# Optimization experiments

Measured on AMD Instinct MI355X. Metric: run time of the kernel, lower is better.

The kernel has to match this reference:

```python
import jax, jax.numpy as jnp
import numpy as np

N_NODES = 100000
N_EDGES = 1600000
D = 128          # h_size == feature_representation_size
N_CLASSES = 2
N_GRAPHS = 64


def setup_inputs() -> dict:
    key = jax.random.key(0)
    ks = jax.random.split(key, 8)
    scale = 1.0 / np.sqrt(D)
    x = jax.random.normal(ks[0], (N_NODES, D), jnp.float32)
    edge_index = jax.random.randint(ks[1], (2, N_EDGES), 0, N_NODES, dtype=jnp.int64)
    batch = jnp.sort(jax.random.randint(ks[2], (N_NODES,), 0, N_GRAPHS, dtype=jnp.int64))
    W0 = jax.random.normal(ks[3], (D, D), jnp.float32) * scale
    W1 = jax.random.normal(ks[4], (D, D), jnp.float32) * scale
    W2 = jax.random.normal(ks[5], (D, D), jnp.float32) * scale
    Wf = jax.random.normal(ks[6], (D, N_CLASSES), jnp.float32) * scale
    return dict(
        x=x, edge_index=edge_index, batch=batch,
        W0=W0, b0=jnp.zeros((D,), jnp.float32),
        W1=W1, b1=jnp.zeros((D,), jnp.float32),
        W2=W2, b2=jnp.zeros((D,), jnp.float32),
        Wf=Wf, bf=jnp.zeros((N_CLASSES,), jnp.float32),
    )


def gcn_norm(edge_index, num_nodes):
    # add self loops, symmetric normalization D^{-1/2} A_hat D^{-1/2}
    src, dst = edge_index[0], edge_index[1]
    loop = jnp.arange(num_nodes, dtype=src.dtype)
    src = jnp.concatenate([src, loop])
    dst = jnp.concatenate([dst, loop])
    ew = jnp.ones(src.shape[0], jnp.float32)
    deg = jax.ops.segment_sum(ew, dst, num_segments=num_nodes)
    dinv = jnp.where(deg > 0, jax.lax.rsqrt(deg), 0.0)
    norm = dinv[src] * dinv[dst]  # [E+N]
    return src, dst, norm


def gcn_conv(h, W, b, src, dst, norm, num_nodes):
    h = h @ W                                   # linear transform
    msg = h[src] * norm[:, None]                # gather + scale over edges
    out = jax.ops.segment_sum(msg, dst, num_segments=num_nodes)  # scatter-add
    return out + b


def reference(x, edge_index, batch, W0, b0, W1, b1, W2, b2, Wf, bf):
    n = x.shape[0]
    src, dst, norm = gcn_norm(edge_index, n)
    h = jax.nn.relu(gcn_conv(x, W0, b0, src, dst, norm, n))
    h = jax.nn.relu(gcn_conv(h, W1, b1, src, dst, norm, n))
    h = gcn_conv(h, W2, b2, src, dst, norm, n)  # last layer, no relu
    pooled = jax.ops.segment_max(h, batch, num_segments=N_GRAPHS)  # global max pool
    return pooled @ Wf + bf
```

## Files before the change

kernel.cpp:

```cpp
#include <hip/hip_runtime.h>
#include <hip/hip_bf16.h>
#include <hip/hip_fp16.h>
#include <float.h>

#define D 128
#define NGRAPHS 64
#define BKSHIFT 9
#define BKNODES 512
#define MAXBK 256
#define PCH 2048

typedef _Float16 h8 __attribute__((ext_vector_type(8)));
typedef float f4 __attribute__((ext_vector_type(4)));

__device__ __forceinline__ unsigned fkey(float f){
  unsigned u = __float_as_uint(f);
  return (u & 0x80000000u) ? ~u : (u | 0x80000000u);
}
__device__ __forceinline__ float funkey(unsigned k){
  unsigned u = (k & 0x80000000u) ? (k ^ 0x80000000u) : ~k;
  return __uint_as_float(u);
}

__device__ __forceinline__ void wcvt_pair(const float* __restrict__ W,
    _Float16* __restrict__ dstp, int pair, int lane){
  int quad = lane >> 4;
  int n    = lane & 15;
  int k0 = pair >> 3;
  int tt = pair & 7;
  _Float16 v[8];
  #pragma unroll
  for (int j = 0; j < 8; j++){
    int k = k0 * 32 + quad * 8 + j;
    v[j] = (_Float16)W[k * 128 + 16 * tt + n];
  }
  *(uint4*)&dstp[((size_t)pair * 64 + lane) * 8] = *(uint4*)v;
}

__global__ __launch_bounds__(256) void k_wcvt0(const float* __restrict__ W0,
    _Float16* __restrict__ Wsw, int* __restrict__ bcnt){
  if (blockIdx.x == 0 && threadIdx.x < MAXBK) bcnt[threadIdx.x] = 0;
  int lane = threadIdx.x & 63;
  int pair = blockIdx.x * 4 + (threadIdx.x >> 6);
  wcvt_pair(W0, Wsw, pair, lane);
}

#define HCH 4096
__global__ __launch_bounds__(256) void k_mega(
    const float* __restrict__ x, const _Float16* __restrict__ Wsw0,
    _Float16* __restrict__ C, int M, int gb,
    const int* __restrict__ dst, int* __restrict__ bcnt, int E, int nh,
    const float* __restrict__ W1, const float* __restrict__ W2,
    _Float16* __restrict__ Wsw12){
  __shared__ __align__(16) char smraw[4 * 16 * 136 * 2];
  int bid = blockIdx.x;
  if (bid < gb){
    _Float16 (*lds)[136] = (_Float16(*)[136])(smraw + (threadIdx.x >> 6) * 16 * 136 * 2);
    int lane = threadIdx.x & 63;
    int quad = lane >> 4;
    int l15  = lane & 15;
    int m0 = bid * 64 + (threadIdx.x >> 6) * 16;
    if (m0 >= M) return;
    f4 acc[8] = {};
    h8 af[4];
    const float* arow = x + (size_t)(m0 + l15) * D;
    #pragma unroll
    for (int k0 = 0; k0 < 4; k0++){
      float4 a = *(const float4*)&arow[k0 * 32 + quad * 8];
      float4 b = *(const float4*)&arow[k0 * 32 + quad * 8 + 4];
      __half2 p0 = __floats2half2_rn(a.x, a.y);
      __half2 p1 = __floats2half2_rn(a.z, a.w);
      __half2 p2 = __floats2half2_rn(b.x, b.y);
      __half2 p3 = __floats2half2_rn(b.z, b.w);
      union { uint4 u; h8 v; } cv;
      cv.u.x = *(unsigned*)&p0; cv.u.y = *(unsigned*)&p1;
      cv.u.z = *(unsigned*)&p2; cv.u.w = *(unsigned*)&p3;
      af[k0] = cv.v;
    }
    #pragma unroll
    for (int k0 = 0; k0 < 4; k0++){
      #pragma unroll
      for (int t = 0; t < 8; t++){
        h8 bf = *(const h8*)&Wsw0[((size_t)(k0 * 8 + t) * 64 + lane) * 8];
        acc[t] = __builtin_amdgcn_mfma_f32_16x16x32_f16(af[k0], bf, acc[t], 0, 0, 0);
      }
    }
    #pragma unroll
    for (int t = 0; t < 8; t++){
      #pragma unroll
      for (int r = 0; r < 4; r++)
        lds[quad * 4 + r][t * 16 + l15] = (_Float16)acc[t][r];
    }
    #pragma unroll
    for (int it = 0; it < 4; it++){
      int idx = it * 64 + lane;
      int row = idx >> 4;
      int ch  = idx & 15;
      *(uint4*)&C[(size_t)(m0 + row) * D + ch * 8] = *(uint4*)&lds[row][ch * 8];
    }
    return;
  }
  bid -= gb;
  if (bid < nh){
    int* h = (int*)smraw;
    int t = threadIdx.x;
    for (int i = t; i < MAXBK; i += 256) h[i] = 0;
    __syncthreads();
    int e0 = bid * HCH;
    #pragma unroll
    for (int j = 0; j < HCH / 256; j++){
      int e = e0 + t + j * 256;
      if (e < E) atomicAdd(&h[dst[e] >> BKSHIFT], 1);
    }
    __syncthreads();
    for (int i = t; i < MAXBK; i += 256) if (h[i]) atomicAdd(&bcnt[i], h[i]);
    return;
  }
  bid -= nh;
  const float* W = (bid < 2) ? W1 : W2;
  _Float16* dstp = Wsw12 + ((bid < 2) ? 0 : 16384);
  int pbase = (bid & 1) * 16;
  int lane = threadIdx.x & 63;
  for (int pp = (threadIdx.x >> 6); pp < 16; pp += 4)
    wcvt_pair(W, dstp, pbase + pp, lane);
}

__global__ __launch_bounds__(256) void k_bscan(const int* __restrict__ bcnt,
    int* __restrict__ bOff, int* __restrict__ bCur, int* __restrict__ row_ptr,
    unsigned* __restrict__ pk, int nbk, int N, int E){
  __shared__ int sh[256];
  int t = threadIdx.x;
  for (int i = t; i < NGRAPHS * D; i += 256) pk[i] = 0u;
  int v = (t < nbk) ? bcnt[t] : 0;
  sh[t] = v; __syncthreads();
  for (int off = 1; off < 256; off <<= 1){
    int x = (t >= off) ? sh[t - off] : 0;
    __syncthreads();
    sh[t] += x;
    __syncthreads();
  }
  if (t < nbk){ int ex = sh[t] - v; bOff[t] = ex; bCur[t] = ex; }
  if (t == 0){ bOff[nbk] = E; row_ptr[N] = E; }
}

__global__ __launch_bounds__(256) void k_part(const int* __restrict__ src,
    const int* __restrict__ dst, int* __restrict__ bCur,
    uint2* __restrict__ epart, int E){
  __shared__ int scnt[MAXBK], soff[MAXBK], sbase[MAXBK], scur[MAXBK];
  __shared__ int stmp[256];
  __shared__ uint2 stage[PCH];
  int t = threadIdx.x;
  int e0 = blockIdx.x * PCH;
  int eN = E - e0; if (eN > PCH) eN = PCH;
  for (int i = t; i < MAXBK; i += 256){ scnt[i] = 0; scur[i] = 0; }
  __syncthreads();
  uint2 mye[PCH / 256];
  #pragma unroll
  for (int j = 0; j < PCH / 256; j++){
    int e = e0 + t + j * 256;
    if (e < E){
      mye[j].x = (unsigned)src[e];
      mye[j].y = (unsigned)dst[e];
      atomicAdd(&scnt[mye[j].y >> BKSHIFT], 1);
    }
  }
  __syncthreads();
  int v = scnt[t];
  stmp[t] = v; __syncthreads();
  for (int off = 1; off < 256; off <<= 1){
    int x = (t >= off) ? stmp[t - off] : 0;
    __syncthreads();
    stmp[t] += x;
    __syncthreads();
  }
  soff[t] = stmp[t] - v;
  if (v > 0) sbase[t] = atomicAdd(&bCur[t], v);
  __syncthreads();
  #pragma unroll
  for (int j = 0; j < PCH / 256; j++){
    int e = e0 + t + j * 256;
    if (e < E){
      int b = mye[j].y >> BKSHIFT;
      int l = atomicAdd(&scur[b], 1);
      stage[soff[b] + l] = mye[j];
    }
  }
  __syncthreads();
  for (int j = t; j < eN; j += 256){
    uint2 ed = stage[j];
    int b = (int)(ed.y >> BKSHIFT);
    epart[(size_t)sbase[b] + (j - soff[b])] = ed;
  }
}

__global__ __launch_bounds__(256) void k_bfill(const uint2* __restrict__ epart,
    const int* __restrict__ bOff, int* __restrict__ row_ptr,
    int* __restrict__ col, float* __restrict__ dinv, int N){
  __shared__ int hc[BKNODES], off[BKNODES], cur[BKNODES];
  __shared__ int stmp[256];
  int b = blockIdx.x, t = threadIdx.x;
  int base = bOff[b], cntE = bOff[b + 1] - base;
  int node0 = b << BKSHIFT;
  int nloc = N - node0; if (nloc > BKNODES) nloc = BKNODES;
  for (int i = t; i < BKNODES; i += 256) hc[i] = 0;
  __syncthreads();
  for (int j = t; j < cntE; j += 256){
    uint2 ed = epart[(size_t)base + j];
    atomicAdd(&hc[ed.y - node0], 1);
  }
  __syncthreads();
  int a0 = hc[2 * t], a1 = hc[2 * t + 1];
  int s = a0 + a1;
  stmp[t] = s; __syncthreads();
  for (int o = 1; o < 256; o <<= 1){
    int x = (t >= o) ? stmp[t - o] : 0;
    __syncthreads();
    stmp[t] += x;
    __syncthreads();
  }
  int ex = stmp[t] - s;
  off[2 * t] = ex; off[2 * t + 1] = ex + a0;
  __syncthreads();
  for (int i = t; i < nloc; i += 256){
    row_ptr[node0 + i] = base + off[i];
    dinv[node0 + i]    = rsqrtf((float)hc[i] + 1.0f);
    cur[i] = off[i];
  }
  __syncthreads();
  for (int j = t; j < cntE; j += 256){
    uint2 ed = epart[(size_t)base + j];
    int p = atomicAdd(&cur[ed.y - node0], 1);
    col[base + p] = (int)ed.x;
  }
}

__global__ __launch_bounds__(256) void gemm_mfma(const _Float16* __restrict__ A,
    const _Float16* __restrict__ Wsw, _Float16* __restrict__ C, int M){
  __shared__ _Float16 lds[4][16][136];
  int wave = threadIdx.x >> 6;
  int lane = threadIdx.x & 63;
  int quad = lane >> 4;
  int l15  = lane & 15;
  int m0 = blockIdx.x * 64 + wave * 16;
  if (m0 >= M) return;
  f4 acc[8] = {};
  h8 af[4];
  const _Float16* arow = A + (size_t)(m0 + l15) * D;
  #pragma unroll
  for (int k0 = 0; k0 < 4; k0++)
    af[k0] = *(const h8*)&arow[k0 * 32 + quad * 8];
  #pragma unroll
  for (int k0 = 0; k0 < 4; k0++){
    #pragma unroll
    for (int t = 0; t < 8; t++){
      h8 bf = *(const h8*)&Wsw[((size_t)(k0 * 8 + t) * 64 + lane) * 8];
      acc[t] = __builtin_amdgcn_mfma_f32_16x16x32_f16(af[k0], bf, acc[t], 0, 0, 0);
    }
  }
  #pragma unroll
  for (int t = 0; t < 8; t++){
    #pragma unroll
    for (int r = 0; r < 4; r++)
      lds[wave][quad * 4 + r][t * 16 + l15] = (_Float16)acc[t][r];
  }
  #pragma unroll
  for (int it = 0; it < 4; it++){
    int idx = it * 64 + lane;
    int row = idx >> 4;
    int ch  = idx & 15;
    *(uint4*)&C[(size_t)(m0 + row) * D + ch * 8] = *(uint4*)&lds[wave][row][ch * 8];
  }
}

__device__ __forceinline__ void accm(float* acc, uint4 u, float w){
  union { uint4 u; _Float16 h[8]; } cv;
  cv.u = u;
  #pragma unroll
  for (int k = 0; k < 8; k++)
    acc[k] += (float)cv.h[k] * w;
}

__global__ __launch_bounds__(256) void k_agg(const __half* __restrict__ t,
    const int* __restrict__ row_ptr, const int* __restrict__ col,
    const float* __restrict__ dinv, const float* __restrict__ bias,
    __half* __restrict__ outh, int relu, int N){
  int node = blockIdx.x * 4 + (threadIdx.x >> 6);
  if (node >= N) return;
  int lane = threadIdx.x & 63;
  int way  = lane >> 4;
  int cg   = (lane & 15) * 8;
  float di = dinv[node];
  int beg = row_ptr[node], end = row_ptr[node + 1];
  float acc[8] = {0.f,0.f,0.f,0.f,0.f,0.f,0.f,0.f};
  int j = beg + way;
  for (; j + 12 < end; j += 16){
    int s0 = col[j], s1 = col[j + 4], s2 = col[j + 8], s3 = col[j + 12];
    float w0 = dinv[s0] * di;
    float w1 = dinv[s1] * di;
    float w2 = dinv[s2] * di;
    float w3 = dinv[s3] * di;
    uint4 u0 = *(const uint4*)&t[(size_t)s0 * D + cg];
    uint4 u1 = *(const uint4*)&t[(size_t)s1 * D + cg];
    uint4 u2 = *(const uint4*)&t[(size_t)s2 * D + cg];
    uint4 u3 = *(const uint4*)&t[(size_t)s3 * D + cg];
    accm(acc, u0, w0);
    accm(acc, u1, w1);
    accm(acc, u2, w2);
    accm(acc, u3, w3);
  }
  for (; j < end; j += 4){
    int s = col[j];
    float w = dinv[s] * di;
    uint4 u = *(const uint4*)&t[(size_t)s * D + cg];
    accm(acc, u, w);
  }
  #pragma unroll
  for (int k = 0; k < 8; k++){
    acc[k] += __shfl_xor(acc[k], 16, 64);
    acc[k] += __shfl_xor(acc[k], 32, 64);
  }
  if (way == 0){
    uint4 su = *(const uint4*)&t[(size_t)node * D + cg];
    union { uint4 u; _Float16 h[8]; } sv; sv.u = su;
    float dii = di * di;
    float4 b0 = *(const float4*)&bias[cg];
    float4 b1 = *(const float4*)&bias[cg + 4];
    float bb[8] = {b0.x, b0.y, b0.z, b0.w, b1.x, b1.y, b1.z, b1.w};
    float o[8];
    #pragma unroll
    for (int k = 0; k < 8; k++)
      o[k] = acc[k] + (float)sv.h[k] * dii + bb[k];
    if (relu){
      #pragma unroll
      for (int k = 0; k < 8; k++) o[k] = fmaxf(o[k], 0.f);
    }
    __half2 p0 = __floats2half2_rn(o[0], o[1]);
    __half2 p1 = __floats2half2_rn(o[2], o[3]);
    __half2 p2 = __floats2half2_rn(o[4], o[5]);
    __half2 p3 = __floats2half2_rn(o[6], o[7]);
    uint4 u;
    u.x = *(unsigned*)&p0; u.y = *(unsigned*)&p1;
    u.z = *(unsigned*)&p2; u.w = *(unsigned*)&p3;
    *(uint4*)&outh[(size_t)node * D + cg] = u;
  }
}

__global__ __launch_bounds__(128) void k_pool(const __half* __restrict__ h,
    const int* __restrict__ batch, unsigned* __restrict__ pk, int N){
  int d = threadIdx.x;
  int n0 = blockIdx.x * 64;
  int nEnd = n0 + 64; if (nEnd > N) nEnd = N;
  float cur = -FLT_MAX;
  int curg = batch[n0];
  int n = n0;
  for (; n + 3 < nEnd; n += 4){
    const __half* r = &h[(size_t)n * D + d];
    __half v0 = r[0], v1 = r[D], v2 = r[2 * D], v3 = r[3 * D];
    int g0 = batch[n], g1 = batch[n + 1], g2 = batch[n + 2], g3 = batch[n + 3];
    if (g0 != curg){ atomicMax(&pk[curg * D + d], fkey(cur)); cur = -FLT_MAX; curg = g0; }
    cur = fmaxf(cur, __half2float(v0));
    if (g1 != curg){ atomicMax(&pk[curg * D + d], fkey(cur)); cur = -FLT_MAX; curg = g1; }
    cur = fmaxf(cur, __half2float(v1));
    if (g2 != curg){ atomicMax(&pk[curg * D + d], fkey(cur)); cur = -FLT_MAX; curg = g2; }
    cur = fmaxf(cur, __half2float(v2));
    if (g3 != curg){ atomicMax(&pk[curg * D + d], fkey(cur)); cur = -FLT_MAX; curg = g3; }
    cur = fmaxf(cur, __half2float(v3));
  }
  for (; n < nEnd; n++){
    int g = batch[n];
    if (g != curg){ atomicMax(&pk[curg * D + d], fkey(cur)); cur = -FLT_MAX; curg = g; }
    cur = fmaxf(cur, __half2float(h[(size_t)n * D + d]));
  }
  atomicMax(&pk[curg * D + d], fkey(cur));
}

__global__ __launch_bounds__(128) void k_final(const unsigned* __restrict__ pk,
    const float* __restrict__ Wf, const float* __restrict__ bf,
    float* __restrict__ out){
  int t = threadIdx.x;
  int g = t >> 1, c = t & 1;
  float s = bf[c];
  for (int k = 0; k < D; k++)
    s += funkey(pk[g * D + k]) * Wf[k * 2 + c];
  out[g * 2 + c] = s;
}

extern "C" void kernel_launch(void* const* d_in, const int* in_sizes, int n_in,
                              void* d_out, int out_size, void* d_ws, size_t ws_size,
                              hipStream_t stream){
  const float* x   = (const float*)d_in[0];
  const int*   ei  = (const int*)d_in[1];
  const int*   bat = (const int*)d_in[2];
  const float* W0  = (const float*)d_in[3];
  const float* b0  = (const float*)d_in[4];
  const float* W1  = (const float*)d_in[5];
  const float* b1  = (const float*)d_in[6];
  const float* W2  = (const float*)d_in[7];
  const float* b2  = (const float*)d_in[8];
  const float* Wf  = (const float*)d_in[9];
  const float* bf  = (const float*)d_in[10];
  int N = in_sizes[0] / D;
  int E = in_sizes[1] / 2;
  const int* srcp = ei;
  const int* dstp = ei + E;
  int nbk   = (N + BKNODES - 1) / BKNODES;
  int npart = (E + PCH - 1) / PCH;
  int nh    = (E + HCH - 1) / HCH;
  int gb    = (N + 63) / 64;

  char* p = (char*)d_ws;
  auto alloc = [&](size_t bytes)->char*{
    char* r = p; p += (bytes + 255) & ~(size_t)255; return r;
  };
  float*     dinv    = (float*)alloc((size_t)N * 4);
  int*       row_ptr = (int*)alloc((size_t)(N + 1) * 4);
  int*       col     = (int*)alloc((size_t)E * 4);
  uint2*     epart   = (uint2*)alloc((size_t)E * 8);
  _Float16*  tmp     = (_Float16*)alloc((size_t)N * D * 2);
  _Float16*  tmp2    = (_Float16*)alloc((size_t)N * D * 2);
  _Float16*  Wsw     = (_Float16*)alloc((size_t)3 * 16384 * 2);
  unsigned*  pk      = (unsigned*)alloc((size_t)NGRAPHS * D * 4);
  int*       bcnt    = (int*)alloc((size_t)MAXBK * 4);
  int*       bOff    = (int*)alloc((size_t)(MAXBK + 1) * 4);
  int*       bCur    = (int*)alloc((size_t)MAXBK * 4);

  k_wcvt0<<<8, 256, 0, stream>>>(W0, Wsw, bcnt);
  k_mega<<<gb + nh + 4, 256, 0, stream>>>(x, Wsw, tmp, N, gb,
      dstp, bcnt, E, nh, W1, W2, Wsw + 16384);
  k_bscan<<<1, 256, 0, stream>>>(bcnt, bOff, bCur, row_ptr, pk, nbk, N, E);
  k_part<<<npart, 256, 0, stream>>>(srcp, dstp, bCur, epart, E);
  k_bfill<<<nbk, 256, 0, stream>>>(epart, bOff, row_ptr, col, dinv, N);

  int ablocks = (N + 3) / 4;
  k_agg<<<ablocks, 256, 0, stream>>>((const __half*)tmp, row_ptr, col, dinv, b0, (__half*)tmp2, 1, N);
  gemm_mfma<<<gb, 256, 0, stream>>>(tmp2, Wsw + 16384, tmp, N);
  k_agg<<<ablocks, 256, 0, stream>>>((const __half*)tmp, row_ptr, col, dinv, b1, (__half*)tmp2, 1, N);
  gemm_mfma<<<gb, 256, 0, stream>>>(tmp2, Wsw + 32768, tmp, N);
  k_agg<<<ablocks, 256, 0, stream>>>((const __half*)tmp, row_ptr, col, dinv, b2, (__half*)tmp2, 0, N);
  k_pool<<<(N + 63) / 64, 128, 0, stream>>>((const __half*)tmp2, bat, pk, N);
  k_final<<<1, 128, 0, stream>>>(pk, Wf, bf, (float*)d_out);
}
```

Before: 411.1 us.

## Fuse aggregation with the next layer's MFMA transform and fuse max-pooling

Layers 2 and 3 now aggregate neighbours first and then multiply by the weight matrix inside one kernel. Each wave aggregates 16 nodes into LDS, runs the MFMA GEMM, and applies bias and ReLU. The final layer max-pools straight from LDS instead of writing the hidden state, which removes the separate GEMM and pool kernels and two full N×D fp16 round trips. The cost is that each wave walks its 16 nodes one after another, so fewer independent gathers are in flight to hide memory latency.

```diff
diff --git a/kernel.cpp b/kernel.cpp
--- a/kernel.cpp
+++ b/kernel.cpp
@@ -231,44 +231,6 @@
     uint2 ed = epart[(size_t)base + j];
     int p = atomicAdd(&cur[ed.y - node0], 1);
     col[base + p] = (int)ed.x;
-  }
-}
-
-__global__ __launch_bounds__(256) void gemm_mfma(const _Float16* __restrict__ A,
-    const _Float16* __restrict__ Wsw, _Float16* __restrict__ C, int M){
-  __shared__ _Float16 lds[4][16][136];
-  int wave = threadIdx.x >> 6;
-  int lane = threadIdx.x & 63;
-  int quad = lane >> 4;
-  int l15  = lane & 15;
-  int m0 = blockIdx.x * 64 + wave * 16;
-  if (m0 >= M) return;
-  f4 acc[8] = {};
-  h8 af[4];
-  const _Float16* arow = A + (size_t)(m0 + l15) * D;
-  #pragma unroll
-  for (int k0 = 0; k0 < 4; k0++)
-    af[k0] = *(const h8*)&arow[k0 * 32 + quad * 8];
-  #pragma unroll
-  for (int k0 = 0; k0 < 4; k0++){
-    #pragma unroll
-    for (int t = 0; t < 8; t++){
-      h8 bf = *(const h8*)&Wsw[((size_t)(k0 * 8 + t) * 64 + lane) * 8];
-      acc[t] = __builtin_amdgcn_mfma_f32_16x16x32_f16(af[k0], bf, acc[t], 0, 0, 0);
-    }
-  }
-  #pragma unroll
-  for (int t = 0; t < 8; t++){
-    #pragma unroll
-    for (int r = 0; r < 4; r++)
-      lds[wave][quad * 4 + r][t * 16 + l15] = (_Float16)acc[t][r];
-  }
-  #pragma unroll
-  for (int it = 0; it < 4; it++){
-    int idx = it * 64 + lane;
-    int row = idx >> 4;
-    int ch  = idx & 15;
-    *(uint4*)&C[(size_t)(m0 + row) * D + ch * 8] = *(uint4*)&lds[wave][row][ch * 8];
   }
 }
 
@@ -345,33 +307,114 @@
   }
 }
 
-__global__ __launch_bounds__(128) void k_pool(const __half* __restrict__ h,
-    const int* __restrict__ batch, unsigned* __restrict__ pk, int N){
-  int d = threadIdx.x;
+__global__ __launch_bounds__(256) void k_aggw(const __half* __restrict__ t,
+    const int* __restrict__ row_ptr, const int* __restrict__ col,
+    const float* __restrict__ dinv, const _Float16* __restrict__ Wsw,
+    const float* __restrict__ bias, _Float16* __restrict__ outh,
+    const int* __restrict__ batch, unsigned* __restrict__ pk,
+    int relu, int dopool, int N){
+  __shared__ _Float16 lds[4][16][136];
+  int wave = threadIdx.x >> 6;
+  int lane = threadIdx.x & 63;
+  int way  = lane >> 4;
+  int l15  = lane & 15;
+  int cg   = l15 * 8;
   int n0 = blockIdx.x * 64;
-  int nEnd = n0 + 64; if (nEnd > N) nEnd = N;
-  float cur = -FLT_MAX;
-  int curg = batch[n0];
-  int n = n0;
-  for (; n + 3 < nEnd; n += 4){
-    const __half* r = &h[(size_t)n * D + d];
-    __half v0 = r[0], v1 = r[D], v2 = r[2 * D], v3 = r[3 * D];
-    int g0 = batch[n], g1 = batch[n + 1], g2 = batch[n + 2], g3 = batch[n + 3];
-    if (g0 != curg){ atomicMax(&pk[curg * D + d], fkey(cur)); cur = -FLT_MAX; curg = g0; }
-    cur = fmaxf(cur, __half2float(v0));
-    if (g1 != curg){ atomicMax(&pk[curg * D + d], fkey(cur)); cur = -FLT_MAX; curg = g1; }
-    cur = fmaxf(cur, __half2float(v1));
-    if (g2 != curg){ atomicMax(&pk[curg * D + d], fkey(cur)); cur = -FLT_MAX; curg = g2; }
-    cur = fmaxf(cur, __half2float(v2));
-    if (g3 != curg){ atomicMax(&pk[curg * D + d], fkey(cur)); cur = -FLT_MAX; curg = g3; }
-    cur = fmaxf(cur, __half2float(v3));
-  }
-  for (; n < nEnd; n++){
-    int g = batch[n];
-    if (g != curg){ atomicMax(&pk[curg * D + d], fkey(cur)); cur = -FLT_MAX; curg = g; }
-    cur = fmaxf(cur, __half2float(h[(size_t)n * D + d]));
-  }
-  atomicMax(&pk[curg * D + d], fkey(cur));
+  int m0 = n0 + wave * 16;
+  bool act = (m0 < N);
+  if (act){
+    for (int i = 0; i < 16; i++){
+      int node = m0 + i;
+      float di = dinv[node];
+      int beg = row_ptr[node], end = row_ptr[node + 1];
+      float acc[8] = {0.f,0.f,0.f,0.f,0.f,0.f,0.f,0.f};
+      int j = beg + way;
+      for (; j + 12 < end; j += 16){
+        int s0 = col[j], s1 = col[j + 4], s2 = col[j + 8], s3 = col[j + 12];
+        float w0 = dinv[s0] * di;
+        float w1 = dinv[s1] * di;
+        float w2 = dinv[s2] * di;
+        float w3 = dinv[s3] * di;
+        uint4 u0 = *(const uint4*)&t[(size_t)s0 * D + cg];
+        uint4 u1 = *(const uint4*)&t[(size_t)s1 * D + cg];
+        uint4 u2 = *(const uint4*)&t[(size_t)s2 * D + cg];
+        uint4 u3 = *(const uint4*)&t[(size_t)s3 * D + cg];
+        accm(acc, u0, w0);
+        accm(acc, u1, w1);
+        accm(acc, u2, w2);
+        accm(acc, u3, w3);
+      }
+      for (; j < end; j += 4){
+        int s = col[j];
+        float w = dinv[s] * di;
+        uint4 u = *(const uint4*)&t[(size_t)s * D + cg];
+        accm(acc, u, w);
+      }
+      #pragma unroll
+      for (int k = 0; k < 8; k++){
+        acc[k] += __shfl_xor(acc[k], 16, 64);
+        acc[k] += __shfl_xor(acc[k], 32, 64);
+      }
+      if (way == 0){
+        uint4 su = *(const uint4*)&t[(size_t)node * D + cg];
+        union { uint4 u; _Float16 h[8]; } sv; sv.u = su;
+        float dii = di * di;
+        _Float16 o[8];
+        #pragma unroll
+        for (int k = 0; k < 8; k++)
+          o[k] = (_Float16)(acc[k] + (float)sv.h[k] * dii);
+        *(uint4*)&lds[wave][i][cg] = *(uint4*)o;
+      }
+    }
+    h8 af[4];
+    #pragma unroll
+    for (int k0 = 0; k0 < 4; k0++)
+      af[k0] = *(const h8*)&lds[wave][l15][k0 * 32 + way * 8];
+    f4 c[8] = {};
+    #pragma unroll
+    for (int k0 = 0; k0 < 4; k0++){
+      #pragma unroll
+      for (int tt = 0; tt < 8; tt++){
+        h8 bfr = *(const h8*)&Wsw[((size_t)(k0 * 8 + tt) * 64 + lane) * 8];
+        c[tt] = __builtin_amdgcn_mfma_f32_16x16x32_f16(af[k0], bfr, c[tt], 0, 0, 0);
+      }
+    }
+    #pragma unroll
+    for (int tt = 0; tt < 8; tt++){
+      float b = bias[tt * 16 + l15];
+      #pragma unroll
+      for (int r = 0; r < 4; r++){
+        float v = c[tt][r] + b;
+        if (relu) v = fmaxf(v, 0.f);
+        lds[wave][way * 4 + r][tt * 16 + l15] = (_Float16)v;
+      }
+    }
+    if (!dopool){
+      #pragma unroll
+      for (int it = 0; it < 4; it++){
+        int idx = it * 64 + lane;
+        int row = idx >> 4;
+        int ch  = idx & 15;
+        if (m0 + row < N)
+          *(uint4*)&outh[(size_t)(m0 + row) * D + ch * 8] = *(uint4*)&lds[wave][row][ch * 8];
+      }
+    }
+  }
+  if (dopool){
+    __syncthreads();
+    if (threadIdx.x < 128){
+      int d = threadIdx.x;
+      int nEnd = N - n0; if (nEnd > 64) nEnd = 64;
+      float cur = -FLT_MAX;
+      int curg = batch[n0];
+      for (int n = 0; n < nEnd; n++){
+        int g = batch[n0 + n];
+        if (g != curg){ atomicMax(&pk[curg * D + d], fkey(cur)); cur = -FLT_MAX; curg = g; }
+        cur = fmaxf(cur, (float)lds[n >> 4][n & 15][d]);
+      }
+      atomicMax(&pk[curg * D + d], fkey(cur));
+    }
+  }
 }
 
 __global__ __launch_bounds__(128) void k_final(const unsigned* __restrict__ pk,
@@ -432,11 +475,11 @@
   k_bfill<<<nbk, 256, 0, stream>>>(epart, bOff, row_ptr, col, dinv, N);
 
   int ablocks = (N + 3) / 4;
+  int fblocks = (N + 63) / 64;
   k_agg<<<ablocks, 256, 0, stream>>>((const __half*)tmp, row_ptr, col, dinv, b0, (__half*)tmp2, 1, N);
-  gemm_mfma<<<gb, 256, 0, stream>>>(tmp2, Wsw + 16384, tmp, N);
-  k_agg<<<ablocks, 256, 0, stream>>>((const __half*)tmp, row_ptr, col, dinv, b1, (__half*)tmp2, 1, N);
-  gemm_mfma<<<gb, 256, 0, stream>>>(tmp2, Wsw + 32768, tmp, N);
-  k_agg<<<ablocks, 256, 0, stream>>>((const __half*)tmp, row_ptr, col, dinv, b2, (__half*)tmp2, 0, N);
-  k_pool<<<(N + 63) / 64, 128, 0, stream>>>((const __half*)tmp2, bat, pk, N);
+  k_aggw<<<fblocks, 256, 0, stream>>>((const __half*)tmp2, row_ptr, col, dinv,
+      Wsw + 16384, b1, tmp, (const int*)nullptr, (unsigned*)nullptr, 1, 0, N);
+  k_aggw<<<fblocks, 256, 0, stream>>>((const __half*)tmp, row_ptr, col, dinv,
+      Wsw + 32768, b2, (_Float16*)nullptr, bat, pk, 0, 1, N);
   k_final<<<1, 128, 0, stream>>>(pk, Wf, bf, (float*)d_out);
 }
```

After: 458.5 us. 1.12x slower.

## Fuse CSR build stages to cut launches and redundant bucket-offset scans

Applied to the files above, without the earlier changes.

Moves the destination-bucket histogram into the W0 conversion kernel and fuses edge partitioning into the mega kernel, which now runs alongside the first GEMM. Each partition block recomputes the bucket prefix scan locally, so the separate single-block scan kernel and the bOff buffer go away. k_bfill now uses 512 threads (one per node in a bucket) and recomputes its bucket base, and a memset zeroes pk/bcnt/bCur. This removes two kernel launches and their serialization, at the cost of redundant per-block scans and larger LDS use in the mega kernel, which may lower occupancy for the GEMM blocks.

```diff
diff --git a/kernel.cpp b/kernel.cpp
--- a/kernel.cpp
+++ b/kernel.cpp
@@ -9,6 +9,7 @@
 #define BKNODES 512
 #define MAXBK 256
 #define PCH 2048
+#define HCH 4096
 
 typedef _Float16 h8 __attribute__((ext_vector_type(8)));
 typedef float f4 __attribute__((ext_vector_type(4)));
@@ -37,22 +38,38 @@
   *(uint4*)&dstp[((size_t)pair * 64 + lane) * 8] = *(uint4*)v;
 }
 
-__global__ __launch_bounds__(256) void k_wcvt0(const float* __restrict__ W0,
-    _Float16* __restrict__ Wsw, int* __restrict__ bcnt){
-  if (blockIdx.x == 0 && threadIdx.x < MAXBK) bcnt[threadIdx.x] = 0;
-  int lane = threadIdx.x & 63;
-  int pair = blockIdx.x * 4 + (threadIdx.x >> 6);
-  wcvt_pair(W0, Wsw, pair, lane);
-}
-
-#define HCH 4096
-__global__ __launch_bounds__(256) void k_mega(
+__global__ __launch_bounds__(256) void k_wcvt0h(const float* __restrict__ W0,
+    _Float16* __restrict__ Wsw, const int* __restrict__ dst,
+    int* __restrict__ bcnt, int E){
+  __shared__ int h[MAXBK];
+  if (blockIdx.x < 8){
+    int lane = threadIdx.x & 63;
+    int pair = blockIdx.x * 4 + (threadIdx.x >> 6);
+    wcvt_pair(W0, Wsw, pair, lane);
+    return;
+  }
+  int t = threadIdx.x;
+  for (int i = t; i < MAXBK; i += 256) h[i] = 0;
+  __syncthreads();
+  int e0 = (blockIdx.x - 8) * HCH;
+  #pragma unroll
+  for (int j = 0; j < HCH / 256; j++){
+    int e = e0 + t + j * 256;
+    if (e < E) atomicAdd(&h[dst[e] >> BKSHIFT], 1);
+  }
+  __syncthreads();
+  for (int i = t; i < MAXBK; i += 256) if (h[i]) atomicAdd(&bcnt[i], h[i]);
+}
+
+__global__ __launch_bounds__(256) void k_mega2(
     const float* __restrict__ x, const _Float16* __restrict__ Wsw0,
     _Float16* __restrict__ C, int M, int gb,
-    const int* __restrict__ dst, int* __restrict__ bcnt, int E, int nh,
+    const int* __restrict__ src, const int* __restrict__ dst,
+    const int* __restrict__ bcnt, int* __restrict__ bCur,
+    uint2* __restrict__ epart, int E, int npart,
     const float* __restrict__ W1, const float* __restrict__ W2,
     _Float16* __restrict__ Wsw12){
-  __shared__ __align__(16) char smraw[4 * 16 * 136 * 2];
+  __shared__ __align__(16) char smraw[5120 + PCH * 8];
   int bid = blockIdx.x;
   if (bid < gb){
     _Float16 (*lds)[136] = (_Float16(*)[136])(smraw + (threadIdx.x >> 6) * 16 * 136 * 2);
@@ -101,22 +118,68 @@
     return;
   }
   bid -= gb;
-  if (bid < nh){
-    int* h = (int*)smraw;
+  if (bid < npart){
+    int* scnt  = (int*)smraw;
+    int* soff  = (int*)(smraw + 1024);
+    int* sbase = (int*)(smraw + 2048);
+    int* scur  = (int*)(smraw + 3072);
+    int* stmp  = (int*)(smraw + 4096);
+    uint2* stage = (uint2*)(smraw + 5120);
     int t = threadIdx.x;
-    for (int i = t; i < MAXBK; i += 256) h[i] = 0;
-    __syncthreads();
-    int e0 = bid * HCH;
-    #pragma unroll
-    for (int j = 0; j < HCH / 256; j++){
+    int bv = bcnt[t];
+    stmp[t] = bv; __syncthreads();
+    for (int off = 1; off < 256; off <<= 1){
+      int xv = (t >= off) ? stmp[t - off] : 0;
+      __syncthreads();
+      stmp[t] += xv;
+      __syncthreads();
+    }
+    int boffl = stmp[t] - bv;
+    __syncthreads();
+    int e0 = bid * PCH;
+    int eN = E - e0; if (eN > PCH) eN = PCH;
+    for (int i = t; i < MAXBK; i += 256){ scnt[i] = 0; scur[i] = 0; }
+    __syncthreads();
+    uint2 mye[PCH / 256];
+    #pragma unroll
+    for (int j = 0; j < PCH / 256; j++){
       int e = e0 + t + j * 256;
-      if (e < E) atomicAdd(&h[dst[e] >> BKSHIFT], 1);
-    }
-    __syncthreads();
-    for (int i = t; i < MAXBK; i += 256) if (h[i]) atomicAdd(&bcnt[i], h[i]);
+      if (e < E){
+        mye[j].x = (unsigned)src[e];
+        mye[j].y = (unsigned)dst[e];
+        atomicAdd(&scnt[mye[j].y >> BKSHIFT], 1);
+      }
+    }
+    __syncthreads();
+    int v = scnt[t];
+    stmp[t] = v; __syncthreads();
+    for (int off = 1; off < 256; off <<= 1){
+      int xv = (t >= off) ? stmp[t - off] : 0;
+      __syncthreads();
+      stmp[t] += xv;
+      __syncthreads();
+    }
+    soff[t] = stmp[t] - v;
+    if (v > 0) sbase[t] = boffl + atomicAdd(&bCur[t], v);
+    __syncthreads();
+    #pragma unroll
+    for (int j = 0; j < PCH / 256; j++){
+      int e = e0 + t + j * 256;
+      if (e < E){
+        int b = mye[j].y >> BKSHIFT;
+        int l = atomicAdd(&scur[b], 1);
+        stage[soff[b] + l] = mye[j];
+      }
+    }
+    __syncthreads();
+    for (int j = t; j < eN; j += 256){
+      uint2 ed = stage[j];
+      int b = (int)(ed.y >> BKSHIFT);
+      epart[(size_t)sbase[b] + (j - soff[b])] = ed;
+    }
     return;
   }
-  bid -= nh;
+  bid -= npart;
   const float* W = (bid < 2) ? W1 : W2;
   _Float16* dstp = Wsw12 + ((bid < 2) ? 0 : 16384);
   int pbase = (bid & 1) * 16;
@@ -125,150 +188,52 @@
     wcvt_pair(W, dstp, pbase + pp, lane);
 }
 
-__global__ __launch_bounds__(256) void k_bscan(const int* __restrict__ bcnt,
-    int* __restrict__ bOff, int* __restrict__ bCur, int* __restrict__ row_ptr,
-    unsigned* __restrict__ pk, int nbk, int N, int E){
-  __shared__ int sh[256];
-  int t = threadIdx.x;
-  for (int i = t; i < NGRAPHS * D; i += 256) pk[i] = 0u;
-  int v = (t < nbk) ? bcnt[t] : 0;
-  sh[t] = v; __syncthreads();
-  for (int off = 1; off < 256; off <<= 1){
-    int x = (t >= off) ? sh[t - off] : 0;
-    __syncthreads();
-    sh[t] += x;
-    __syncthreads();
-  }
-  if (t < nbk){ int ex = sh[t] - v; bOff[t] = ex; bCur[t] = ex; }
-  if (t == 0){ bOff[nbk] = E; row_ptr[N] = E; }
-}
-
-__global__ __launch_bounds__(256) void k_part(const int* __restrict__ src,
-    const int* __restrict__ dst, int* __restrict__ bCur,
-    uint2* __restrict__ epart, int E){
-  __shared__ int scnt[MAXBK], soff[MAXBK], sbase[MAXBK], scur[MAXBK];
-  __shared__ int stmp[256];
-  __shared__ uint2 stage[PCH];
-  int t = threadIdx.x;
-  int e0 = blockIdx.x * PCH;
-  int eN = E - e0; if (eN > PCH) eN = PCH;
-  for (int i = t; i < MAXBK; i += 256){ scnt[i] = 0; scur[i] = 0; }
-  __syncthreads();
-  uint2 mye[PCH / 256];
-  #pragma unroll
-  for (int j = 0; j < PCH / 256; j++){
-    int e = e0 + t + j * 256;
-    if (e < E){
-      mye[j].x = (unsigned)src[e];
-      mye[j].y = (unsigned)dst[e];
-      atomicAdd(&scnt[mye[j].y >> BKSHIFT], 1);
-    }
-  }
-  __syncthreads();
-  int v = scnt[t];
-  stmp[t] = v; __syncthreads();
-  for (int off = 1; off < 256; off <<= 1){
-    int x = (t >= off) ? stmp[t - off] : 0;
-    __syncthreads();
-    stmp[t] += x;
-    __syncthreads();
-  }
-  soff[t] = stmp[t] - v;
-  if (v > 0) sbase[t] = atomicAdd(&bCur[t], v);
-  __syncthreads();
-  #pragma unroll
-  for (int j = 0; j < PCH / 256; j++){
-    int e = e0 + t + j * 256;
-    if (e < E){
-      int b = mye[j].y >> BKSHIFT;
-      int l = atomicAdd(&scur[b], 1);
-      stage[soff[b] + l] = mye[j];
-    }
-  }
-  __syncthreads();
-  for (int j = t; j < eN; j += 256){
-    uint2 ed = stage[j];
-    int b = (int)(ed.y >> BKSHIFT);
-    epart[(size_t)sbase[b] + (j - soff[b])] = ed;
-  }
-}
-
-__global__ __launch_bounds__(256) void k_bfill(const uint2* __restrict__ epart,
-    const int* __restrict__ bOff, int* __restrict__ row_ptr,
-    int* __restrict__ col, float* __restrict__ dinv, int N){
-  __shared__ int hc[BKNODES], off[BKNODES], cur[BKNODES];
-  __shared__ int stmp[256];
+__global__ __launch_bounds__(512) void k_bfill(const uint2* __restrict__ epart,
+    const int* __restrict__ bcnt, int* __restrict__ row_ptr,
+    int* __restrict__ col, float* __restrict__ dinv, int N, int E){
+  __shared__ int hc[BKNODES], cur[BKNODES];
+  __shared__ int stmp[512];
   int b = blockIdx.x, t = threadIdx.x;
-  int base = bOff[b], cntE = bOff[b + 1] - base;
+  int bv = (t < MAXBK) ? bcnt[t] : 0;
+  stmp[t] = bv; __syncthreads();
+  for (int o = 1; o < 512; o <<= 1){
+    int xv = (t >= o) ? stmp[t - o] : 0;
+    __syncthreads();
+    stmp[t] += xv;
+    __syncthreads();
+  }
+  int cntE = bcnt[b];
+  int base = stmp[b] - cntE;
+  __syncthreads();
+  if (b == (int)gridDim.x - 1 && t == 0) row_ptr[N] = E;
   int node0 = b << BKSHIFT;
   int nloc = N - node0; if (nloc > BKNODES) nloc = BKNODES;
-  for (int i = t; i < BKNODES; i += 256) hc[i] = 0;
-  __syncthreads();
-  for (int j = t; j < cntE; j += 256){
+  hc[t] = 0;
+  __syncthreads();
+  for (int j = t; j < cntE; j += 512){
     uint2 ed = epart[(size_t)base + j];
     atomicAdd(&hc[ed.y - node0], 1);
   }
   __syncthreads();
-  int a0 = hc[2 * t], a1 = hc[2 * t + 1];
-  int s = a0 + a1;
+  int s = hc[t];
   stmp[t] = s; __syncthreads();
-  for (int o = 1; o < 256; o <<= 1){
-    int x = (t >= o) ? stmp[t - o] : 0;
-    __syncthreads();
-    stmp[t] += x;
+  for (int o = 1; o < 512; o <<= 1){
+    int xv = (t >= o) ? stmp[t - o] : 0;
+    __syncthreads();
+    stmp[t] += xv;
     __syncthreads();
   }
   int ex = stmp[t] - s;
-  off[2 * t] = ex; off[2 * t + 1] = ex + a0;
-  __syncthreads();
-  for (int i = t; i < nloc; i += 256){
-    row_ptr[node0 + i] = base + off[i];
-    dinv[node0 + i]    = rsqrtf((float)hc[i] + 1.0f);
-    cur[i] = off[i];
-  }
-  __syncthreads();
-  for (int j = t; j < cntE; j += 256){
+  if (t < nloc){
+    row_ptr[node0 + t] = base + ex;
+    dinv[node0 + t]    = rsqrtf((float)s + 1.0f);
+  }
+  cur[t] = ex;
+  __syncthreads();
+  for (int j = t; j < cntE; j += 512){
     uint2 ed = epart[(size_t)base + j];
     int p = atomicAdd(&cur[ed.y - node0], 1);
     col[base + p] = (int)ed.x;
-  }
-}
-
-__global__ __launch_bounds__(256) void gemm_mfma(const _Float16* __restrict__ A,
-    const _Float16* __restrict__ Wsw, _Float16* __restrict__ C, int M){
-  __shared__ _Float16 lds[4][16][136];
-  int wave = threadIdx.x >> 6;
-  int lane = threadIdx.x & 63;
-  int quad = lane >> 4;
-  int l15  = lane & 15;
-  int m0 = blockIdx.x * 64 + wave * 16;
-  if (m0 >= M) return;
-  f4 acc[8] = {};
-  h8 af[4];
-  const _Float16* arow = A + (size_t)(m0 + l15) * D;
-  #pragma unroll
-  for (int k0 = 0; k0 < 4; k0++)
-    af[k0] = *(const h8*)&arow[k0 * 32 + quad * 8];
-  #pragma unroll
-  for (int k0 = 0; k0 < 4; k0++){
-    #pragma unroll
-    for (int t = 0; t < 8; t++){
-      h8 bf = *(const h8*)&Wsw[((size_t)(k0 * 8 + t) * 64 + lane) * 8];
-      acc[t] = __builtin_amdgcn_mfma_f32_16x16x32_f16(af[k0], bf, acc[t], 0, 0, 0);
-    }
-  }
-  #pragma unroll
-  for (int t = 0; t < 8; t++){
-    #pragma unroll
-    for (int r = 0; r < 4; r++)
-      lds[wave][quad * 4 + r][t * 16 + l15] = (_Float16)acc[t][r];
-  }
-  #pragma unroll
-  for (int it = 0; it < 4; it++){
-    int idx = it * 64 + lane;
-    int row = idx >> 4;
-    int ch  = idx & 15;
-    *(uint4*)&C[(size_t)(m0 + row) * D + ch * 8] = *(uint4*)&lds[wave][row][ch * 8];
   }
 }
 
@@ -345,6 +310,44 @@
   }
 }
 
+__global__ __launch_bounds__(256) void gemm_mfma(const _Float16* __restrict__ A,
+    const _Float16* __restrict__ Wsw, _Float16* __restrict__ C, int M){
+  __shared__ _Float16 lds[4][16][136];
+  int wave = threadIdx.x >> 6;
+  int lane = threadIdx.x & 63;
+  int quad = lane >> 4;
+  int l15  = lane & 15;
+  int m0 = blockIdx.x * 64 + wave * 16;
+  if (m0 >= M) return;
+  f4 acc[8] = {};
+  h8 af[4];
+  const _Float16* arow = A + (size_t)(m0 + l15) * D;
+  #pragma unroll
+  for (int k0 = 0; k0 < 4; k0++)
+    af[k0] = *(const h8*)&arow[k0 * 32 + quad * 8];
+  #pragma unroll
+  for (int k0 = 0; k0 < 4; k0++){
+    #pragma unroll
+    for (int t = 0; t < 8; t++){
+      h8 bf = *(const h8*)&Wsw[((size_t)(k0 * 8 + t) * 64 + lane) * 8];
+      acc[t] = __builtin_amdgcn_mfma_f32_16x16x32_f16(af[k0], bf, acc[t], 0, 0, 0);
+    }
+  }
+  #pragma unroll
+  for (int t = 0; t < 8; t++){
+    #pragma unroll
+    for (int r = 0; r < 4; r++)
+      lds[wave][quad * 4 + r][t * 16 + l15] = (_Float16)acc[t][r];
+  }
+  #pragma unroll
+  for (int it = 0; it < 4; it++){
+    int idx = it * 64 + lane;
+    int row = idx >> 4;
+    int ch  = idx & 15;
+    *(uint4*)&C[(size_t)(m0 + row) * D + ch * 8] = *(uint4*)&lds[wave][row][ch * 8];
+  }
+}
+
 __global__ __launch_bounds__(128) void k_pool(const __half* __restrict__ h,
     const int* __restrict__ batch, unsigned* __restrict__ pk, int N){
   int d = threadIdx.x;
@@ -421,15 +424,13 @@
   _Float16*  Wsw     = (_Float16*)alloc((size_t)3 * 16384 * 2);
   unsigned*  pk      = (unsigned*)alloc((size_t)NGRAPHS * D * 4);
   int*       bcnt    = (int*)alloc((size_t)MAXBK * 4);
-  int*       bOff    = (int*)alloc((size_t)(MAXBK + 1) * 4);
   int*       bCur    = (int*)alloc((size_t)MAXBK * 4);
 
-  k_wcvt0<<<8, 256, 0, stream>>>(W0, Wsw, bcnt);
-  k_mega<<<gb + nh + 4, 256, 0, stream>>>(x, Wsw, tmp, N, gb,
-      dstp, bcnt, E, nh, W1, W2, Wsw + 16384);
-  k_bscan<<<1, 256, 0, stream>>>(bcnt, bOff, bCur, row_ptr, pk, nbk, N, E);
-  k_part<<<npart, 256, 0, stream>>>(srcp, dstp, bCur, epart, E);
-  k_bfill<<<nbk, 256, 0, stream>>>(epart, bOff, row_ptr, col, dinv, N);
+  hipMemsetAsync(pk, 0, 32768 + 1024 + 1024, stream);
+  k_wcvt0h<<<8 + nh, 256, 0, stream>>>(W0, Wsw, dstp, bcnt, E);
+  k_mega2<<<gb + npart + 4, 256, 0, stream>>>(x, Wsw, tmp, N, gb,
+      srcp, dstp, bcnt, bCur, epart, E, npart, W1, W2, Wsw + 16384);
+  k_bfill<<<nbk, 512, 0, stream>>>(epart, bcnt, row_ptr, col, dinv, N, E);
 
   int ablocks = (N + 3) / 4;
   k_agg<<<ablocks, 256, 0, stream>>>((const __half*)tmp, row_ptr, col, dinv, b0, (__half*)tmp2, 1, N);
```

Result: faster. 400.2 us (-2.7%).
